# Kernel tuning notes

Measured on AMD Instinct MI355X. Metric: run time of the kernel, lower is better.

The kernel has to match this reference:

```python
import jax, jax.numpy as jnp
import numpy as np

EPS = 1e-12  # F.normalize eps

def _l2_normalize(x):
    n = jnp.linalg.norm(x, axis=-1, keepdims=True)
    return x / jnp.maximum(n, EPS)

def setup_inputs() -> dict:
    key = jax.random.key(0)
    k1, k2 = jax.random.split(key)
    B, C, F = 32768, 1000, 256
    features = jax.random.normal(k1, (B, F), dtype=jnp.float32)
    prototypes = jax.random.normal(k2, (C, F), dtype=jnp.float32)
    distance_scale = jnp.ones((1,), dtype=jnp.float32)
    temperature = jnp.ones((1,), dtype=jnp.float32)
    return {"features": features, "prototypes": prototypes,
            "distance_scale": distance_scale, "temperature": temperature}

def reference(features, prototypes, distance_scale, temperature):
    # Normalize both sides to the unit sphere (F.normalize, p=2, eps=1e-12)
    fn = _l2_normalize(features)       # [B, F]
    pn = _l2_normalize(prototypes)     # [C, F]
    # For unit vectors: ||a-b||_2 / sqrt(2) = sqrt(1 - a.b)
    cos = jnp.einsum('bf,cf->bc', fn, pn)          # [B, C]
    dist = jnp.sqrt(jnp.maximum(1.0 - cos, 0.0))   # cdist(...)/sqrt(2)
    iso = jnp.abs(distance_scale[0]) * dist
    logits = -(iso + jnp.mean(iso, axis=1, keepdims=True))
    return logits / temperature[0]
```

## Files before the change

### kernel.cpp

```cpp
#include <hip/hip_runtime.h>


typedef __attribute__((ext_vector_type(8))) short short8;
typedef __attribute__((ext_vector_type(4))) float f32x4;
typedef __fp16 h2 __attribute__((ext_vector_type(2)));

union U16 { uint4 u4; short8 s8; };

static __device__ __forceinline__ unsigned short f2bf(float x){
  union { float f; unsigned u; } v; v.f = x;
  unsigned r = v.u + 0x7fffu + ((v.u >> 16) & 1u);
  return (unsigned short)(r >> 16);
}

#define CPAD 1024

__global__ void norm_protos_kernel(const float* __restrict__ src,
                                   unsigned short* __restrict__ dst, int C)
{
  const int wave = threadIdx.x >> 6;
  const int lane = threadIdx.x & 63;
  const int row  = blockIdx.x * 4 + wave;
  const int t    = row >> 4;
  const int l16  = row & 15;
  const int s    = lane >> 3;
  const int quad = (lane >> 1) & 3;
  const int j    = (lane & 1) * 4;

  ushort4 o = {0, 0, 0, 0};
  if (row < C){
    const float4 v = *(const float4*)(src + row * 256 + lane * 4);
    float ss = v.x*v.x + v.y*v.y + v.z*v.z + v.w*v.w;
    #pragma unroll
    for (int off = 32; off; off >>= 1) ss += __shfl_xor(ss, off);
    const float inv = 1.0f / fmaxf(sqrtf(ss), 1e-12f);
    o.x = f2bf(v.x * inv); o.y = f2bf(v.y * inv);
    o.z = f2bf(v.z * inv); o.w = f2bf(v.w * inv);
  }
  *(ushort4*)(dst + ((size_t)((t*8 + s)*64 + quad*16 + l16))*8 + j) = o;
}

__global__ __launch_bounds__(256, 3)
void fused_kernel(const float* __restrict__ feats,
                  const unsigned short* __restrict__ pnw,
                  const float* __restrict__ ds,
                  const float* __restrict__ temp,
                  float* __restrict__ out, int C)
{
  __shared__ float wsum[16][4];

  const int tid  = threadIdx.x;
  const int wave = tid >> 6;
  const int lane = tid & 63;
  const int quad = lane >> 4;
  const int l16  = lane & 15;
  const long rowbase = (long)blockIdx.x * 16;

  short8 ffrag[8];
  {
    const float* rp = feats + (rowbase + l16) * 256 + quad*8;
    float4 va[8], vb[8];
    float ss = 0.f;
    #pragma unroll
    for (int s = 0; s < 8; ++s){
      va[s] = *(const float4*)(rp + s*32);
      vb[s] = *(const float4*)(rp + s*32 + 4);
      ss += va[s].x*va[s].x + va[s].y*va[s].y + va[s].z*va[s].z + va[s].w*va[s].w;
      ss += vb[s].x*vb[s].x + vb[s].y*vb[s].y + vb[s].z*vb[s].z + vb[s].w*vb[s].w;
    }
    ss += __shfl_xor(ss, 16);
    ss += __shfl_xor(ss, 32);
    const float inv = __builtin_amdgcn_rcpf(__builtin_amdgcn_sqrtf(fmaxf(ss, 1e-24f)));
    #pragma unroll
    for (int s = 0; s < 8; ++s){
      U16 u;
      u.u4.x = (unsigned)f2bf(va[s].x*inv) | ((unsigned)f2bf(va[s].y*inv) << 16);
      u.u4.y = (unsigned)f2bf(va[s].z*inv) | ((unsigned)f2bf(va[s].w*inv) << 16);
      u.u4.z = (unsigned)f2bf(vb[s].x*inv) | ((unsigned)f2bf(vb[s].y*inv) << 16);
      u.u4.w = (unsigned)f2bf(vb[s].z*inv) | ((unsigned)f2bf(vb[s].w*inv) << 16);
      ffrag[s] = u.s8;
    }
  }

  const uint4* tp = (const uint4*)pnw + (size_t)(wave*16)*512 + lane;

  h2 dd[16][2];
  float rsum = 0.f;

  #pragma unroll
  for (int wt = 0; wt < 16; ++wt){
    const uint4* bp = tp + (size_t)wt*512;
    short8 pfrag[8];
    #pragma unroll
    for (int s = 0; s < 8; ++s){ U16 u; u.u4 = bp[s*64]; pfrag[s] = u.s8; }

    f32x4 acc = (f32x4){0.f, 0.f, 0.f, 0.f};
    #pragma unroll
    for (int s = 0; s < 8; ++s)
      acc = __builtin_amdgcn_mfma_f32_16x16x32_bf16(pfrag[s], ffrag[s], acc, 0, 0, 0);

    float d0 = __builtin_amdgcn_sqrtf(fmaxf(1.0f - acc[0], 0.0f));
    float d1 = __builtin_amdgcn_sqrtf(fmaxf(1.0f - acc[1], 0.0f));
    float d2 = __builtin_amdgcn_sqrtf(fmaxf(1.0f - acc[2], 0.0f));
    float d3 = __builtin_amdgcn_sqrtf(fmaxf(1.0f - acc[3], 0.0f));

    const int cls = wave*256 + wt*16 + quad*4;
    rsum += (cls < C) ? (d0 + d1 + d2 + d3) : 0.0f;

    dd[wt][0] = __builtin_amdgcn_cvt_pkrtz(d0, d1);
    dd[wt][1] = __builtin_amdgcn_cvt_pkrtz(d2, d3);
  }

  rsum += __shfl_xor(rsum, 16);
  rsum += __shfl_xor(rsum, 32);
  if (quad == 0) wsum[l16][wave] = rsum;
  __syncthreads();

  const float4 wv = *(const float4*)&wsum[l16][0];
  const float mean = (wv.x + wv.y + wv.z + wv.w) / (float)C;
  const float nscale = -fabsf(ds[0]) / temp[0];
  const float bias = nscale * mean;

  float* orow = out + (rowbase + l16) * (size_t)C;
  #pragma unroll
  for (int wt = 0; wt < 16; ++wt){
    const int cls = wave*256 + wt*16 + quad*4;
    if (cls < C){
      float4 o;
      o.x = fmaf(nscale, (float)dd[wt][0][0], bias);
      o.y = fmaf(nscale, (float)dd[wt][0][1], bias);
      o.z = fmaf(nscale, (float)dd[wt][1][0], bias);
      o.w = fmaf(nscale, (float)dd[wt][1][1], bias);
      *(float4*)(orow + cls) = o;
    }
  }
}

extern "C" void kernel_launch(void* const* d_in, const int* in_sizes, int n_in,
                              void* d_out, int out_size, void* d_ws, size_t ws_size,
                              hipStream_t stream) {
  const float* features = (const float*)d_in[0];
  const float* protos   = (const float*)d_in[1];
  const float* dscale   = (const float*)d_in[2];
  const float* temp     = (const float*)d_in[3];
  float* out = (float*)d_out;

  const int F = 256;
  const int B = in_sizes[0] / F;
  const int C = in_sizes[1] / F;

  unsigned short* pnw = (unsigned short*)d_ws;

  norm_protos_kernel<<<CPAD/4, 256, 0, stream>>>(protos, pnw, C);
  fused_kernel<<<B/16, 256, 0, stream>>>(features, pnw, dscale, temp, out, C);
}
```

Before: 207.3 us.

## Process 32 rows per block with 8 waves, reusing prototype fragments across two row groups

Each block now handles 32 feature rows with 512 threads. Each of the 8 waves covers 128 classes instead of 256 and multiplies every loaded prototype fragment against two 16-row feature groups. The aim is to halve prototype fragment reloads per output row and to spread the work over more waves. The cost is more registers per thread (two feature-fragment sets and two accumulators) under a tighter launch bound of 512 threads at occupancy 4, which could cause spills. The cross-wave mean reduction in shared memory is rebuilt for 8 waves and 32 rows.

```diff
diff --git a/kernel.cpp b/kernel.cpp
--- a/kernel.cpp
+++ b/kernel.cpp
@@ -37,28 +37,29 @@
     o.x = f2bf(v.x * inv); o.y = f2bf(v.y * inv);
     o.z = f2bf(v.z * inv); o.w = f2bf(v.w * inv);
   }
-  *(ushort4*)(dst + ((size_t)((t*8 + s)*64 + quad*16 + l16))*8 + j) = o;
+  *(ushort4*)(dst + ((size_t)(t*512 + s*64 + quad*16 + l16))*8 + j) = o;
 }
 
-__global__ __launch_bounds__(256, 3)
+__global__ __launch_bounds__(512, 4)
 void fused_kernel(const float* __restrict__ feats,
                   const unsigned short* __restrict__ pnw,
                   const float* __restrict__ ds,
                   const float* __restrict__ temp,
                   float* __restrict__ out, int C)
 {
-  __shared__ float wsum[16][4];
+  __shared__ float wsum[8][32];
 
   const int tid  = threadIdx.x;
   const int wave = tid >> 6;
   const int lane = tid & 63;
   const int quad = lane >> 4;
   const int l16  = lane & 15;
-  const long rowbase = (long)blockIdx.x * 16;
+  const long rowbase = (long)blockIdx.x * 32;
 
-  short8 ffrag[8];
-  {
-    const float* rp = feats + (rowbase + l16) * 256 + quad*8;
+  short8 ffrag[2][8];
+  #pragma unroll
+  for (int g = 0; g < 2; ++g){
+    const float* rp = feats + (rowbase + g*16 + l16) * 256 + quad*8;
     float4 va[8], vb[8];
     float ss = 0.f;
     #pragma unroll
@@ -78,60 +79,92 @@
       u.u4.y = (unsigned)f2bf(va[s].z*inv) | ((unsigned)f2bf(va[s].w*inv) << 16);
       u.u4.z = (unsigned)f2bf(vb[s].x*inv) | ((unsigned)f2bf(vb[s].y*inv) << 16);
       u.u4.w = (unsigned)f2bf(vb[s].z*inv) | ((unsigned)f2bf(vb[s].w*inv) << 16);
-      ffrag[s] = u.s8;
+      ffrag[g][s] = u.s8;
     }
   }
 
-  const uint4* tp = (const uint4*)pnw + (size_t)(wave*16)*512 + lane;
+  const uint4* tp = (const uint4*)pnw + (size_t)(wave*8)*512 + lane;
 
-  h2 dd[16][2];
-  float rsum = 0.f;
+  h2 dd[2][8][2];
+  float rsum0 = 0.f, rsum1 = 0.f;
 
   #pragma unroll
-  for (int wt = 0; wt < 16; ++wt){
+  for (int wt = 0; wt < 8; ++wt){
     const uint4* bp = tp + (size_t)wt*512;
     short8 pfrag[8];
     #pragma unroll
     for (int s = 0; s < 8; ++s){ U16 u; u.u4 = bp[s*64]; pfrag[s] = u.s8; }
 
-    f32x4 acc = (f32x4){0.f, 0.f, 0.f, 0.f};
+    f32x4 acc0 = (f32x4){0.f,0.f,0.f,0.f};
+    f32x4 acc1 = (f32x4){0.f,0.f,0.f,0.f};
     #pragma unroll
-    for (int s = 0; s < 8; ++s)
-      acc = __builtin_amdgcn_mfma_f32_16x16x32_bf16(pfrag[s], ffrag[s], acc, 0, 0, 0);
+    for (int s = 0; s < 8; ++s){
+      acc0 = __builtin_amdgcn_mfma_f32_16x16x32_bf16(pfrag[s], ffrag[0][s], acc0, 0, 0, 0);
+      acc1 = __builtin_amdgcn_mfma_f32_16x16x32_bf16(pfrag[s], ffrag[1][s], acc1, 0, 0, 0);
+    }
 
-    float d0 = __builtin_amdgcn_sqrtf(fmaxf(1.0f - acc[0], 0.0f));
-    float d1 = __builtin_amdgcn_sqrtf(fmaxf(1.0f - acc[1], 0.0f));
-    float d2 = __builtin_amdgcn_sqrtf(fmaxf(1.0f - acc[2], 0.0f));
-    float d3 = __builtin_amdgcn_sqrtf(fmaxf(1.0f - acc[3], 0.0f));
+    const int cls = wave*128 + wt*16 + quad*4;
+    const bool valid = cls < C;
 
-    const int cls = wave*256 + wt*16 + quad*4;
-    rsum += (cls < C) ? (d0 + d1 + d2 + d3) : 0.0f;
+    float a0 = __builtin_amdgcn_sqrtf(fmaxf(1.0f - acc0[0], 0.0f));
+    float a1 = __builtin_amdgcn_sqrtf(fmaxf(1.0f - acc0[1], 0.0f));
+    float a2 = __builtin_amdgcn_sqrtf(fmaxf(1.0f - acc0[2], 0.0f));
+    float a3 = __builtin_amdgcn_sqrtf(fmaxf(1.0f - acc0[3], 0.0f));
+    float b0 = __builtin_amdgcn_sqrtf(fmaxf(1.0f - acc1[0], 0.0f));
+    float b1 = __builtin_amdgcn_sqrtf(fmaxf(1.0f - acc1[1], 0.0f));
+    float b2 = __builtin_amdgcn_sqrtf(fmaxf(1.0f - acc1[2], 0.0f));
+    float b3 = __builtin_amdgcn_sqrtf(fmaxf(1.0f - acc1[3], 0.0f));
 
-    dd[wt][0] = __builtin_amdgcn_cvt_pkrtz(d0, d1);
-    dd[wt][1] = __builtin_amdgcn_cvt_pkrtz(d2, d3);
+    rsum0 += valid ? (a0 + a1 + a2 + a3) : 0.0f;
+    rsum1 += valid ? (b0 + b1 + b2 + b3) : 0.0f;
+
+    dd[0][wt][0] = __builtin_amdgcn_cvt_pkrtz(a0, a1);
+    dd[0][wt][1] = __builtin_amdgcn_cvt_pkrtz(a2, a3);
+    dd[1][wt][0] = __builtin_amdgcn_cvt_pkrtz(b0, b1);
+    dd[1][wt][1] = __builtin_amdgcn_cvt_pkrtz(b2, b3);
   }
 
-  rsum += __shfl_xor(rsum, 16);
-  rsum += __shfl_xor(rsum, 32);
-  if (quad == 0) wsum[l16][wave] = rsum;
+  rsum0 += __shfl_xor(rsum0, 16);
+  rsum0 += __shfl_xor(rsum0, 32);
+  rsum1 += __shfl_xor(rsum1, 16);
+  rsum1 += __shfl_xor(rsum1, 32);
+  if (quad == 0){
+    wsum[wave][l16]      = rsum0;
+    wsum[wave][16 + l16] = rsum1;
+  }
   __syncthreads();
 
-  const float4 wv = *(const float4*)&wsum[l16][0];
-  const float mean = (wv.x + wv.y + wv.z + wv.w) / (float)C;
+  const float invC = 1.0f / (float)C;
+  float mean0 = 0.f, mean1 = 0.f;
+  #pragma unroll
+  for (int w = 0; w < 8; ++w){
+    mean0 += wsum[w][l16];
+    mean1 += wsum[w][16 + l16];
+  }
+  mean0 *= invC; mean1 *= invC;
+
   const float nscale = -fabsf(ds[0]) / temp[0];
-  const float bias = nscale * mean;
+  const float bias0 = nscale * mean0;
+  const float bias1 = nscale * mean1;
 
-  float* orow = out + (rowbase + l16) * (size_t)C;
+  float* orow0 = out + (rowbase + l16) * (size_t)C;
+  float* orow1 = out + (rowbase + 16 + l16) * (size_t)C;
   #pragma unroll
-  for (int wt = 0; wt < 16; ++wt){
-    const int cls = wave*256 + wt*16 + quad*4;
+  for (int wt = 0; wt < 8; ++wt){
+    const int cls = wave*128 + wt*16 + quad*4;
     if (cls < C){
       float4 o;
-      o.x = fmaf(nscale, (float)dd[wt][0][0], bias);
-      o.y = fmaf(nscale, (float)dd[wt][0][1], bias);
-      o.z = fmaf(nscale, (float)dd[wt][1][0], bias);
-      o.w = fmaf(nscale, (float)dd[wt][1][1], bias);
-      *(float4*)(orow + cls) = o;
+      o.x = fmaf(nscale, (float)dd[0][wt][0][0], bias0);
+      o.y = fmaf(nscale, (float)dd[0][wt][0][1], bias0);
+      o.z = fmaf(nscale, (float)dd[0][wt][1][0], bias0);
+      o.w = fmaf(nscale, (float)dd[0][wt][1][1], bias0);
+      *(float4*)(orow0 + cls) = o;
+      float4 p;
+      p.x = fmaf(nscale, (float)dd[1][wt][0][0], bias1);
+      p.y = fmaf(nscale, (float)dd[1][wt][0][1], bias1);
+      p.z = fmaf(nscale, (float)dd[1][wt][1][0], bias1);
+      p.w = fmaf(nscale, (float)dd[1][wt][1][1], bias1);
+      *(float4*)(orow1 + cls) = p;
     }
   }
 }
@@ -152,5 +185,5 @@
   unsigned short* pnw = (unsigned short*)d_ws;
 
   norm_protos_kernel<<<CPAD/4, 256, 0, stream>>>(protos, pnw, C);
-  fused_kernel<<<B/16, 256, 0, stream>>>(features, pnw, dscale, temp, out, C);
+  fused_kernel<<<B/32, 512, 0, stream>>>(features, pnw, dscale, temp, out, C);
 }
```

Result: slower. 249.9 us (+20.6%).
